# Kernel optimization log

Hardware: AMD Instinct MI355X
Metric: run time of the kernel (lower is better)

The kernel has to match this reference:

```python
import jax, jax.numpy as jnp
import numpy as np

L, C, F, K = 8192, 2048, 128, 257  # timesteps, input_size, filter_size, lag (odd => symmetric 'same' pad)
NY = 256  # number of overwritten channel rows


def setup_inputs() -> dict:
    key = jax.random.key(0)
    k1, k2, k3, k4 = jax.random.split(key, 4)
    x = jax.random.normal(k1, (L, C), dtype=jnp.float32)
    Yt = jax.random.randint(k2, (NY,), 0, C)
    # learned parameters (torch.rand -> uniform[0,1))
    g = jax.random.uniform(k3, (C, F), dtype=jnp.float32)
    kernel = jax.random.uniform(k4, (F, K), dtype=jnp.float32)
    return {"x": x, "Yt": Yt, "g": g, "kernel": kernel}


def reference(x, Yt, g, kernel):
    # synapse[c] is the per-channel 1D filter; the original builds a dense
    # (C, C, K) kernel whose only non-zero slices are the diagonal, so the
    # full conv1d is mathematically a depthwise (grouped) conv.
    synapse = jnp.matmul(g, kernel)          # (C, K)
    lhs = x.T[None]                          # (1, C, L)  NCH
    rhs = synapse[:, None, :]                # (C, 1, K)  OIH, groups=C
    pad = (kernel.shape[1] - 1) // 2         # torch padding='same', odd K
    out = jax.lax.conv_general_dilated(
        lhs, rhs,
        window_strides=(1,),
        padding=[(pad, pad)],
        feature_group_count=x.shape[1],
        dimension_numbers=("NCH", "OIH", "NCH"),
    )                                        # (1, C, L)
    # result[:, Yt, :] = x.T[Yt] : scatter-overwrite selected channel rows
    out = out.at[:, Yt, :].set(x.T[Yt][None])
    return out
```

## Files before the change

### kernel.cpp

```cpp
#include <hip/hip_runtime.h>

#define LL   8192
#define CC   2048
#define FF   128
#define KK   257
#define PAD  128

#define XROW 8448
#define SROW 320
#define NT   18
#define SPLIT 2
#define TILES 4

typedef __bf16 bf16x8 __attribute__((ext_vector_type(8)));
typedef float  f32x16 __attribute__((ext_vector_type(16)));

static __device__ __forceinline__ unsigned short f2bf(float f) {
    unsigned u = __float_as_uint(f);
    u = (u + 0x7fffu + ((u >> 16) & 1u)) >> 16;
    return (unsigned short)u;
}

__global__ __launch_bounds__(256) void synb_kernel(const float* __restrict__ g,
                                                   const float* __restrict__ kern,
                                                   const int* __restrict__ Yt, int ny,
                                                   unsigned short* __restrict__ synEb) {
    __shared__ int sfl[4];
    const int c0 = blockIdx.x * 4;
    const int t  = threadIdx.x;
    if (t < 4) sfl[t] = 0;
    __syncthreads();
    for (int i = t; i < ny; i += 256) {
        int y = Yt[i];
        #pragma unroll
        for (int ii = 0; ii < 4; ++ii) if (y == c0 + ii) sfl[ii] = 1;
    }
    __syncthreads();
    const float* g0 = g + (size_t)(c0 + 0) * FF;
    const float* g1 = g + (size_t)(c0 + 1) * FF;
    const float* g2 = g + (size_t)(c0 + 2) * FF;
    const float* g3 = g + (size_t)(c0 + 3) * FF;
    const int fl0 = sfl[0], fl1 = sfl[1], fl2 = sfl[2], fl3 = sfl[3];
    for (int p = t; p < SROW; p += 256) {
        const int kk = p - 32;
        float a0 = 0.f, a1 = 0.f, a2 = 0.f, a3 = 0.f;
        const bool inr = (kk >= 0) && (kk < KK);
        if (inr) {
            #pragma unroll 8
            for (int f = 0; f < FF; ++f) {
                float kv = kern[f * KK + kk];
                a0 += kv * g0[f];
                a1 += kv * g1[f];
                a2 += kv * g2[f];
                a3 += kv * g3[f];
            }
        }
        float dlt = (kk == PAD) ? 1.f : 0.f;
        float v0 = inr ? (fl0 ? dlt : a0) : 0.f;
        float v1 = inr ? (fl1 ? dlt : a1) : 0.f;
        float v2 = inr ? (fl2 ? dlt : a2) : 0.f;
        float v3 = inr ? (fl3 ? dlt : a3) : 0.f;
        synEb[(size_t)(c0 + 0) * SROW + p] = f2bf(v0);
        synEb[(size_t)(c0 + 1) * SROW + p] = f2bf(v1);
        synEb[(size_t)(c0 + 2) * SROW + p] = f2bf(v2);
        synEb[(size_t)(c0 + 3) * SROW + p] = f2bf(v3);
    }
}

__global__ __launch_bounds__(256) void xpose_kernel(const float* __restrict__ x,
                                                    unsigned short* __restrict__ xbp) {
    __shared__ float tile[64][65];
    const int l0 = blockIdx.x << 6;
    const int c0 = blockIdx.y << 6;
    const int t  = threadIdx.x;
    const int cl = t & 63, ls = t >> 6;
    #pragma unroll
    for (int k = 0; k < 16; ++k) {
        int ll = (k << 2) + ls;
        tile[ll][cl] = x[(size_t)(l0 + ll) * CC + c0 + cl];
    }
    __syncthreads();
    const int lw = (t & 15) << 2, cg = t >> 4;
    #pragma unroll
    for (int k = 0; k < 4; ++k) {
        int cc = (k << 4) + cg;
        ushort4 v;
        v.x = f2bf(tile[lw + 0][cc]);
        v.y = f2bf(tile[lw + 1][cc]);
        v.z = f2bf(tile[lw + 2][cc]);
        v.w = f2bf(tile[lw + 3][cc]);
        *(ushort4*)(xbp + (size_t)(c0 + cc) * XROW + PAD + l0 + lw) = v;
    }
    if (blockIdx.x == 0) {
        for (int k = 0; k < 32; ++k) {
            int idx = (k << 8) + t, ch = idx >> 7, p = idx & 127;
            xbp[(size_t)(c0 + ch) * XROW + p] = 0;
        }
    } else if (blockIdx.x == 127) {
        for (int k = 0; k < 32; ++k) {
            int idx = (k << 8) + t, ch = idx >> 7, p = idx & 127;
            xbp[(size_t)(c0 + ch) * XROW + PAD + LL + p] = 0;
        }
    }
}

__global__ __launch_bounds__(256, 3) void conv_mfma(const unsigned short* __restrict__ xbp,
                                                    const unsigned short* __restrict__ synEb,
                                                    float* __restrict__ out) {
    __shared__ int4 xw[2][4][192];
    __shared__ unsigned short synL[4][SROW];
    const int w  = threadIdx.x >> 6;
    const int ln = threadIdx.x & 63;
    const int sp = blockIdx.x;
    const int c  = (blockIdx.y << 2) + w;
    const int j  = ln & 31;
    const int q  = ln >> 5;

    {
        const unsigned short* srow = synEb + (size_t)c * SROW;
        #pragma unroll
        for (int k = 0; k < 5; ++k) synL[w][ln + 64 * k] = srow[ln + 64 * k];
    }

    const unsigned short* xrow = xbp + (size_t)c * XROW + (size_t)(sp << 12);
    int4 st0, st1, st2;
    {
        const int4* src = (const int4*)xrow;
        st0 = src[ln];
        st1 = src[ln + 64];
        if (ln < 32) st2 = src[ln + 128];
        int g0 = ln,      s0 = g0 ^ ((g0 >> 3) & 7);
        int g1 = ln + 64, s1 = g1 ^ ((g1 >> 3) & 7);
        xw[0][w][s0] = st0;
        xw[0][w][s1] = st1;
        if (ln < 32) { int g2 = ln + 128, s2 = g2 ^ ((g2 >> 3) & 7); xw[0][w][s2] = st2; }
    }

    bf16x8 bfrag[NT];
    #pragma unroll
    for (int m = 0; m < NT; ++m) {
        union { unsigned short u[8]; bf16x8 v; } B;
        #pragma unroll
        for (int r = 0; r < 8; ++r)
            B.u[r] = synL[w][16 * m + 8 * q + r - j + 32];
        bfrag[m] = B.v;
    }

    const int gb = 4 * j + q;
    float* orow = out + (size_t)c * (size_t)LL + (sp << 12) + j;

    for (int lt = 0; lt < TILES; ++lt) {
        const int buf = lt & 1;
        if (lt < TILES - 1) {
            const int4* src = (const int4*)(xrow + ((lt + 1) << 10));
            st0 = src[ln];
            st1 = src[ln + 64];
            if (ln < 32) st2 = src[ln + 128];
        }
        f32x16 acc;
        #pragma unroll
        for (int r = 0; r < 16; ++r) acc[r] = 0.0f;
        #pragma unroll
        for (int m = 0; m < NT; ++m) {
            int gm = gb + 2 * m;
            union { int4 i4; bf16x8 v; } A;
            A.i4 = xw[buf][w][gm ^ ((gm >> 3) & 7)];
            acc = __builtin_amdgcn_mfma_f32_32x32x16_bf16(A.v, bfrag[m], acc, 0, 0, 0);
        }
        float* o = orow + (lt << 10);
        #pragma unroll
        for (int r = 0; r < 16; ++r) {
            int row = (r & 3) + ((r >> 2) << 3) + (q << 2);
            o[row << 5] = acc[r];
        }
        if (lt < TILES - 1) {
            int g0 = ln,      s0 = g0 ^ ((g0 >> 3) & 7);
            int g1 = ln + 64, s1 = g1 ^ ((g1 >> 3) & 7);
            xw[buf ^ 1][w][s0] = st0;
            xw[buf ^ 1][w][s1] = st1;
            if (ln < 32) { int g2 = ln + 128, s2 = g2 ^ ((g2 >> 3) & 7); xw[buf ^ 1][w][s2] = st2; }
        }
    }
}

extern "C" void kernel_launch(void* const* d_in, const int* in_sizes, int n_in,
                              void* d_out, int out_size, void* d_ws, size_t ws_size,
                              hipStream_t stream) {
    const float* x    = (const float*)d_in[0];
    const int*   Yt   = (const int*)  d_in[1];
    const float* g    = (const float*)d_in[2];
    const float* kern = (const float*)d_in[3];
    float* out = (float*)d_out;
    const int ny = in_sizes[1];

    const size_t xbp_bytes = (size_t)CC * XROW * sizeof(unsigned short);
    unsigned short* xbp   = (unsigned short*)d_ws;
    unsigned short* synEb = (unsigned short*)((char*)d_ws + xbp_bytes);

    synb_kernel<<<CC / 4, 256, 0, stream>>>(g, kern, Yt, ny, synEb);
    xpose_kernel<<<dim3(LL / 64, CC / 64), 256, 0, stream>>>(x, xbp);
    conv_mfma<<<dim3(SPLIT, CC / 4), 256, 0, stream>>>(xbp, synEb, out);
}
```

Measured before the change: 152.2 us.

## Fuse transpose and bf16 conversion into the MFMA depthwise conv kernel

Removes the separate transpose kernel and its bf16 intermediate buffer in global memory. Each block now loads a 16-channel by 1024-timestep window of x, with halo, directly from the row-major input, converts it to bf16 and writes it into swizzled shared memory. Four waves then each run MFMA over four channels. Synapse B-fragments are built from packed 32-bit shared loads using funnel shifts. This drops one launch and a round trip through the intermediate, at the cost of halo overfetch and less double-buffered overlap.

```diff
diff --git a/kernel.cpp b/kernel.cpp
--- a/kernel.cpp
+++ b/kernel.cpp
@@ -6,11 +6,11 @@
 #define KK   257
 #define PAD  128
 
-#define XROW 8448
 #define SROW 320
 #define NT   18
-#define SPLIT 2
-#define TILES 4
+
+#define ROWS 1288
+#define SRP  328
 
 typedef __bf16 bf16x8 __attribute__((ext_vector_type(8)));
 typedef float  f32x16 __attribute__((ext_vector_type(16)));
@@ -67,118 +67,87 @@
     }
 }
 
-__global__ __launch_bounds__(256) void xpose_kernel(const float* __restrict__ x,
-                                                    unsigned short* __restrict__ xbp) {
-    __shared__ float tile[64][65];
-    const int l0 = blockIdx.x << 6;
-    const int c0 = blockIdx.y << 6;
+__global__ __launch_bounds__(256) void fused_conv(const float* __restrict__ x,
+                                                  const unsigned short* __restrict__ synEb,
+                                                  float* __restrict__ out) {
+    __shared__ alignas(16) unsigned short xch[16][ROWS];
+    __shared__ alignas(16) unsigned short synL[16][SRP];
     const int t  = threadIdx.x;
-    const int cl = t & 63, ls = t >> 6;
+    const int W0 = blockIdx.x << 10;
+    const int c0 = blockIdx.y << 4;
+
+    {
+        const int rw = t >> 4;
+        const int u  = t & 15;
+        const unsigned* src = (const unsigned*)(synEb + (size_t)(c0 + rw) * SROW);
+        unsigned* dst = (unsigned*)(synL[rw]);
+        #pragma unroll
+        for (int k = 0; k < 10; ++k) dst[u + (k << 4)] = src[u + (k << 4)];
+    }
+
     #pragma unroll
-    for (int k = 0; k < 16; ++k) {
-        int ll = (k << 2) + ls;
-        tile[ll][cl] = x[(size_t)(l0 + ll) * CC + c0 + cl];
+    for (int k = 0; k < 10; ++k) {
+        int pidx = (k << 8) + t;
+        int ch4  = pidx & 3;
+        int pp   = pidx >> 2;
+        int lg   = W0 + (pp << 1) - 128;
+        const float* sp = x + (size_t)lg * CC + c0 + (ch4 << 2);
+        float4 ve = make_float4(0.f, 0.f, 0.f, 0.f);
+        float4 vo = make_float4(0.f, 0.f, 0.f, 0.f);
+        if ((unsigned)lg       < (unsigned)LL) ve = *(const float4*)sp;
+        if ((unsigned)(lg + 1) < (unsigned)LL) vo = *(const float4*)(sp + CC);
+        int gq = pp >> 2;
+        int gp = gq ^ ((gq >> 3) & 7);
+        int dw = (gp << 2) | (pp & 3);
+        const float* pe = (const float*)&ve;
+        const float* po = (const float*)&vo;
+        #pragma unroll
+        for (int c2 = 0; c2 < 4; ++c2) {
+            unsigned val = (unsigned)f2bf(pe[c2]) | ((unsigned)f2bf(po[c2]) << 16);
+            ((unsigned*)xch[(ch4 << 2) + c2])[dw] = val;
+        }
     }
     __syncthreads();
-    const int lw = (t & 15) << 2, cg = t >> 4;
-    #pragma unroll
-    for (int k = 0; k < 4; ++k) {
-        int cc = (k << 4) + cg;
-        ushort4 v;
-        v.x = f2bf(tile[lw + 0][cc]);
-        v.y = f2bf(tile[lw + 1][cc]);
-        v.z = f2bf(tile[lw + 2][cc]);
-        v.w = f2bf(tile[lw + 3][cc]);
-        *(ushort4*)(xbp + (size_t)(c0 + cc) * XROW + PAD + l0 + lw) = v;
-    }
-    if (blockIdx.x == 0) {
-        for (int k = 0; k < 32; ++k) {
-            int idx = (k << 8) + t, ch = idx >> 7, p = idx & 127;
-            xbp[(size_t)(c0 + ch) * XROW + p] = 0;
-        }
-    } else if (blockIdx.x == 127) {
-        for (int k = 0; k < 32; ++k) {
-            int idx = (k << 8) + t, ch = idx >> 7, p = idx & 127;
-            xbp[(size_t)(c0 + ch) * XROW + PAD + LL + p] = 0;
-        }
-    }
-}
 
-__global__ __launch_bounds__(256, 3) void conv_mfma(const unsigned short* __restrict__ xbp,
-                                                    const unsigned short* __restrict__ synEb,
-                                                    float* __restrict__ out) {
-    __shared__ int4 xw[2][4][192];
-    __shared__ unsigned short synL[4][SROW];
-    const int w  = threadIdx.x >> 6;
-    const int ln = threadIdx.x & 63;
-    const int sp = blockIdx.x;
-    const int c  = (blockIdx.y << 2) + w;
-    const int j  = ln & 31;
-    const int q  = ln >> 5;
+    const int w = t >> 6, ln = t & 63;
+    const int j = ln & 31, q = ln >> 5;
+    const int bb  = (q << 4) - 2 * j + 64;
+    const int dwb = bb >> 2;
+    const int sh  = (bb & 2) << 3;
+    const int gb  = (j << 2) + q;
 
-    {
-        const unsigned short* srow = synEb + (size_t)c * SROW;
+    for (int cc = 0; cc < 4; ++cc) {
+        const int ci = (w << 2) + cc;
+        bf16x8 bfrag[NT];
+        const unsigned* rp = (const unsigned*)(synL[ci]);
         #pragma unroll
-        for (int k = 0; k < 5; ++k) synL[w][ln + 64 * k] = srow[ln + 64 * k];
-    }
-
-    const unsigned short* xrow = xbp + (size_t)c * XROW + (size_t)(sp << 12);
-    int4 st0, st1, st2;
-    {
-        const int4* src = (const int4*)xrow;
-        st0 = src[ln];
-        st1 = src[ln + 64];
-        if (ln < 32) st2 = src[ln + 128];
-        int g0 = ln,      s0 = g0 ^ ((g0 >> 3) & 7);
-        int g1 = ln + 64, s1 = g1 ^ ((g1 >> 3) & 7);
-        xw[0][w][s0] = st0;
-        xw[0][w][s1] = st1;
-        if (ln < 32) { int g2 = ln + 128, s2 = g2 ^ ((g2 >> 3) & 7); xw[0][w][s2] = st2; }
-    }
-
-    bf16x8 bfrag[NT];
-    #pragma unroll
-    for (int m = 0; m < NT; ++m) {
-        union { unsigned short u[8]; bf16x8 v; } B;
-        #pragma unroll
-        for (int r = 0; r < 8; ++r)
-            B.u[r] = synL[w][16 * m + 8 * q + r - j + 32];
-        bfrag[m] = B.v;
-    }
-
-    const int gb = 4 * j + q;
-    float* orow = out + (size_t)c * (size_t)LL + (sp << 12) + j;
-
-    for (int lt = 0; lt < TILES; ++lt) {
-        const int buf = lt & 1;
-        if (lt < TILES - 1) {
-            const int4* src = (const int4*)(xrow + ((lt + 1) << 10));
-            st0 = src[ln];
-            st1 = src[ln + 64];
-            if (ln < 32) st2 = src[ln + 128];
+        for (int m = 0; m < NT; ++m) {
+            int base = dwb + (m << 3);
+            unsigned w0 = rp[base + 0], w1 = rp[base + 1], w2 = rp[base + 2],
+                     w3 = rp[base + 3], w4 = rp[base + 4];
+            union { unsigned d[4]; bf16x8 v; } B;
+            B.d[0] = (unsigned)((((unsigned long long)w1 << 32) | w0) >> sh);
+            B.d[1] = (unsigned)((((unsigned long long)w2 << 32) | w1) >> sh);
+            B.d[2] = (unsigned)((((unsigned long long)w3 << 32) | w2) >> sh);
+            B.d[3] = (unsigned)((((unsigned long long)w4 << 32) | w3) >> sh);
+            bfrag[m] = B.v;
         }
         f32x16 acc;
         #pragma unroll
-        for (int r = 0; r < 16; ++r) acc[r] = 0.0f;
+        for (int r = 0; r < 16; ++r) acc[r] = 0.f;
         #pragma unroll
         for (int m = 0; m < NT; ++m) {
-            int gm = gb + 2 * m;
+            int gq = gb + (m << 1);
+            int gp = gq ^ ((gq >> 3) & 7);
             union { int4 i4; bf16x8 v; } A;
-            A.i4 = xw[buf][w][gm ^ ((gm >> 3) & 7)];
+            A.i4 = *(const int4*)(&xch[ci][gp << 3]);
             acc = __builtin_amdgcn_mfma_f32_32x32x16_bf16(A.v, bfrag[m], acc, 0, 0, 0);
         }
-        float* o = orow + (lt << 10);
+        float* o = out + (size_t)(c0 + ci) * LL + W0 + j;
         #pragma unroll
         for (int r = 0; r < 16; ++r) {
             int row = (r & 3) + ((r >> 2) << 3) + (q << 2);
             o[row << 5] = acc[r];
-        }
-        if (lt < TILES - 1) {
-            int g0 = ln,      s0 = g0 ^ ((g0 >> 3) & 7);
-            int g1 = ln + 64, s1 = g1 ^ ((g1 >> 3) & 7);
-            xw[buf ^ 1][w][s0] = st0;
-            xw[buf ^ 1][w][s1] = st1;
-            if (ln < 32) { int g2 = ln + 128, s2 = g2 ^ ((g2 >> 3) & 7); xw[buf ^ 1][w][s2] = st2; }
         }
     }
 }
@@ -193,11 +162,8 @@
     float* out = (float*)d_out;
     const int ny = in_sizes[1];
 
-    const size_t xbp_bytes = (size_t)CC * XROW * sizeof(unsigned short);
-    unsigned short* xbp   = (unsigned short*)d_ws;
-    unsigned short* synEb = (unsigned short*)((char*)d_ws + xbp_bytes);
+    unsigned short* synEb = (unsigned short*)d_ws;
 
     synb_kernel<<<CC / 4, 256, 0, stream>>>(g, kern, Yt, ny, synEb);
-    xpose_kernel<<<dim3(LL / 64, CC / 64), 256, 0, stream>>>(x, xbp);
-    conv_mfma<<<dim3(SPLIT, CC / 4), 256, 0, stream>>>(xbp, synEb, out);
+    fused_conv<<<dim3(LL / 1024, CC / 16), 256, 0, stream>>>(x, synEb, out);
 }
```

Result: faster. 147.8 us (-2.9%).
